# Optimization experiments

Measured on AMD Instinct MI355X. Metric: run time of the kernel, lower is better.

## Reference

```python
import jax, jax.numpy as jnp
import numpy as np

B, S, EMB, HID, IMG, ATT, K, HL = 64, 512, 768, 512, 2048, 512, 6, 20


def setup_inputs() -> dict:
    key = jax.random.key(0)
    ks = jax.random.split(key, 14)
    u = lambda k, shape: jax.random.uniform(k, shape, jnp.float32, -0.1, 0.1)
    return {
        "representations": jax.random.normal(ks[0], (B, S, EMB), jnp.float32),
        "lengths": jax.random.randint(ks[1], (B,), 0, S),
        "separate_images": jax.random.normal(ks[2], (B, K, IMG), jnp.float32),
        "visual_context": jax.random.normal(ks[3], (B, K * IMG), jnp.float32),
        "prev_hist": jax.random.normal(ks[4], (B, K, HL, EMB), jnp.float32),
        "hist_counts": jax.random.randint(ks[5], (B, K), 0, HL + 1),
        "masks": jax.random.randint(ks[6], (B, S, 1), 0, 2).astype(bool),
        "W_sep": u(ks[7], (IMG, HID)), "b_sep": jnp.zeros((HID,), jnp.float32),
        "W_e2h": u(ks[8], (EMB, HID)), "b_e2h": jnp.zeros((HID,), jnp.float32),
        "W_hist": u(ks[9], (EMB, HID)), "b_hist": jnp.zeros((HID,), jnp.float32),
        "W_ctx": u(ks[10], (K * IMG, HID)), "b_ctx": jnp.zeros((HID,), jnp.float32),
        "W_mm": u(ks[11], (2 * HID, HID)), "b_mm": jnp.zeros((HID,), jnp.float32),
        "W_a1": u(ks[12], (HID, ATT)), "b_a1": jnp.zeros((ATT,), jnp.float32),
        "W_a2": u(ks[13], (ATT, 1)), "b_a2": jnp.zeros((1,), jnp.float32),
    }


def reference(representations, lengths, separate_images, visual_context,
              prev_hist, hist_counts, masks,
              W_sep, b_sep, W_e2h, b_e2h, W_hist, b_hist, W_ctx, b_ctx,
              W_mm, b_mm, W_a1, b_a1, W_a2, b_a2):
    # dropout_prob = 0 -> dropout is identity (eval-mode equivalence)
    input_reps = jax.nn.relu(representations @ W_e2h + b_e2h)          # [B,S,H]
    ctx = jax.nn.relu(visual_context @ W_ctx + b_ctx)                  # [B,H]
    ctx_rep = jnp.broadcast_to(ctx[:, None, :], input_reps.shape)
    mm = jax.nn.relu(jnp.concatenate([input_reps, ctx_rep], -1) @ W_mm + b_mm)  # [B,S,H]
    scores = jnp.tanh(mm @ W_a1 + b_a1) @ W_a2 + b_a2                  # [B,S,1]
    scores = jnp.where(masks, -jnp.inf, scores)
    att_w = jax.nn.softmax(scores, axis=1)                             # softmax over seq
    attended = jnp.sum(mm * att_w, axis=1)                             # [B,H]

    sep = separate_images @ W_sep + b_sep                              # [B,K,H]
    hl = prev_hist.shape[2]
    valid = jnp.arange(hl)[None, None, :] < hist_counts[:, :, None]    # [B,K,HL]
    hsum = jnp.sum(prev_hist * valid[..., None].astype(prev_hist.dtype), axis=2)
    havg = hsum / jnp.maximum(hist_counts, 1)[..., None].astype(prev_hist.dtype)
    hproj = jax.nn.relu(havg @ W_hist + b_hist)                        # [B,K,H]
    sep = sep + jnp.where((hist_counts > 0)[..., None], hproj, 0.0)
    sep = jax.nn.relu(sep)
    # F.normalize(p=2, dim=2, eps=1e-12)
    sep = sep / jnp.maximum(jnp.linalg.norm(sep, axis=2, keepdims=True), 1e-12)
    dot = jnp.einsum('bkh,bh->bk', sep, attended)[..., None]           # [B,K,1]
    return dot
```

## Files before the change

### kernel.cpp

```cpp
#include <hip/hip_runtime.h>
#include <math.h>

#define B_    64
#define S_    512
#define EMB_  768
#define HID_  512
#define IMG_  2048
#define ATT_  512
#define K_    6
#define HL_   20
#define MS_   (B_ * S_)

typedef __attribute__((ext_vector_type(8))) short bf16x8;
typedef __attribute__((ext_vector_type(4))) float f32x4;

__device__ __forceinline__ unsigned short f2b(float f) {
    unsigned int u = __float_as_uint(f);
    u += 0x7fffu + ((u >> 16) & 1u);
    return (unsigned short)(u >> 16);
}
__device__ __forceinline__ unsigned int pk_bf16(float lo, float hi) {
    unsigned int r;
    asm volatile("v_cvt_pk_bf16_f32 %0, %1, %2" : "=v"(r) : "v"(lo), "v"(hi));
    return r;
}

#define GLD_LDS16(gp, lp)                                                        \
    __builtin_amdgcn_global_load_lds(                                            \
        (const __attribute__((address_space(1))) void*)(gp),                     \
        (__attribute__((address_space(3))) void*)(lp), 16, 0, 0)

__global__ __launch_bounds__(256)
void prep(const float* __restrict__ W_e2h, const float* __restrict__ W_mm,
          const float* __restrict__ W_a1,
          unsigned short* __restrict__ WtE2H, unsigned short* __restrict__ WtMM,
          unsigned short* __restrict__ WtA1,
          const unsigned char* __restrict__ masks, int* __restrict__ flag) {
    const int z = blockIdx.z;
    if (z == 3) {
        if (blockIdx.x != 0 || blockIdx.y != 0) return;
        __shared__ int found;
        if (threadIdx.x == 0) found = 0;
        __syncthreads();
        for (int i = threadIdx.x; i < 8192; i += 256)
            if ((i & 3) != 0 && masks[i] != 0) found = 1;
        __syncthreads();
        if (threadIdx.x == 0) *flag = found;
        return;
    }
    const float* W;
    unsigned short* Wt;
    int Kd;
    if (z == 0)      { W = W_e2h; Wt = WtE2H; Kd = EMB_; }
    else if (z == 1) { W = W_mm;  Wt = WtMM;  Kd = HID_; }
    else             { W = W_a1;  Wt = WtA1;  Kd = HID_; }
    if ((int)blockIdx.x * 32 >= Kd) return;

    __shared__ float tile[32][33];
    int k0 = blockIdx.x * 32, n0 = blockIdx.y * 32;
    int tx = threadIdx.x & 31, ty = threadIdx.x >> 5;
    #pragma unroll
    for (int i = 0; i < 4; ++i)
        tile[ty + i * 8][tx] = W[(size_t)(k0 + ty + i * 8) * HID_ + n0 + tx];
    __syncthreads();
    #pragma unroll
    for (int i = 0; i < 4; ++i)
        Wt[(size_t)(n0 + ty + i * 8) * Kd + k0 + tx] = f2b(tile[tx][ty + i * 8]);
}

template<bool AF32, int ACT, bool SCORE>
__global__ __launch_bounds__(512)
void gemm256(const void* __restrict__ Av, const unsigned short* __restrict__ Bt,
             const float* __restrict__ bias, const float* __restrict__ row_add,
             int row_div, unsigned short* __restrict__ Co,
             const float* __restrict__ W_a2, float* __restrict__ scores8,
             int M, int N, int Kd) {
    __shared__ unsigned short Als[2][256 * 64];
    __shared__ unsigned short Bls[2][256 * 64];
    const int tid = threadIdx.x;

    const int nwg = gridDim.x;
    const int cpx = nwg >> 3;
    const int lid = ((int)blockIdx.x & 7) * cpx + ((int)blockIdx.x >> 3);
    const int ntl = N >> 8;
    const int bn = (lid % ntl) << 8;
    const int bm = (lid / ntl) << 8;

    const int lane = tid & 63, wid = tid >> 6;
    const int wr = wid >> 2, wc = wid & 3;
    const int fr = lane & 15, hi = lane >> 4;

    const unsigned short* Ab = (const unsigned short*)Av;
    const float* Af = (const float*)Av;

    f32x4 acc[8][4] = {};

    int srow[4], lcol[4], scol[4];
    #pragma unroll
    for (int c = 0; c < 4; ++c) {
        int g = c * 512 + tid;
        srow[c] = g >> 3;
        lcol[c] = g & 7;
        scol[c] = lcol[c] ^ (srow[c] & 7);
    }

    float4 ra[8];

    auto stageA_lds = [&](int t, int buf) {
        #pragma unroll
        for (int c = 0; c < 4; ++c) {
            int g = c * 512 + tid;
            GLD_LDS16(Ab + (size_t)(bm + srow[c]) * Kd + t * 64 + scol[c] * 8,
                      &Als[buf][g * 8]);
        }
    };
    auto stageB_lds = [&](int t, int buf) {
        #pragma unroll
        for (int c = 0; c < 4; ++c) {
            int g = c * 512 + tid;
            GLD_LDS16(Bt + (size_t)(bn + srow[c]) * Kd + t * 64 + scol[c] * 8,
                      &Bls[buf][g * 8]);
        }
    };
    auto loadA = [&](int t) {
        #pragma unroll
        for (int c = 0; c < 4; ++c) {
            const float* p = Af + (size_t)(bm + srow[c]) * Kd + t * 64 + scol[c] * 8;
            ra[2 * c]     = *(const float4*)p;
            ra[2 * c + 1] = *(const float4*)(p + 4);
        }
    };
    auto writeA = [&](int buf) {
        #pragma unroll
        for (int c = 0; c < 4; ++c) {
            int g = c * 512 + tid;
            uint4 u;
            u.x = pk_bf16(ra[2*c].x,   ra[2*c].y);
            u.y = pk_bf16(ra[2*c].z,   ra[2*c].w);
            u.z = pk_bf16(ra[2*c+1].x, ra[2*c+1].y);
            u.w = pk_bf16(ra[2*c+1].z, ra[2*c+1].w);
            *(uint4*)&Als[buf][g * 8] = u;
        }
    };
    auto compute = [&](int buf) {
        #pragma unroll
        for (int kk = 0; kk < 2; ++kk) {
            bf16x8 af[8], bv[4];
            #pragma unroll
            for (int m = 0; m < 8; ++m) {
                int r = wr * 128 + m * 16 + fr;
                int sc = (kk * 4 + hi) ^ (r & 7);
                af[m] = *(const bf16x8*)&Als[buf][r * 64 + sc * 8];
            }
            #pragma unroll
            for (int n = 0; n < 4; ++n) {
                int r = wc * 64 + n * 16 + fr;
                int sc = (kk * 4 + hi) ^ (r & 7);
                bv[n] = *(const bf16x8*)&Bls[buf][r * 64 + sc * 8];
            }
            #pragma unroll
            for (int m = 0; m < 8; ++m)
                #pragma unroll
                for (int n = 0; n < 4; ++n)
                    acc[m][n] = __builtin_amdgcn_mfma_f32_16x16x32_bf16(af[m], bv[n], acc[m][n], 0, 0, 0);
        }
    };

    const int nt = Kd >> 6;

    if constexpr (AF32) {
        loadA(0);
        stageB_lds(0, 0);
        writeA(0);
    } else {
        stageA_lds(0, 0);
        stageB_lds(0, 0);
    }
    __syncthreads();

    for (int t = 0; t < nt; ++t) {
        const int buf = t & 1;
        const bool pf = (t + 1 < nt);
        if (pf) {
            if constexpr (AF32) {
                loadA(t + 1);
                stageB_lds(t + 1, buf ^ 1);
            } else {
                stageA_lds(t + 1, buf ^ 1);
                stageB_lds(t + 1, buf ^ 1);
            }
        }
        compute(buf);
        if constexpr (AF32) {
            if (pf) writeA(buf ^ 1);
        }
        __syncthreads();
    }

    if (SCORE) {
        float ba[4], wa[4];
        #pragma unroll
        for (int n = 0; n < 4; ++n) {
            int col = bn + wc * 64 + n * 16 + fr;
            ba[n] = bias[col];
            wa[n] = W_a2[col];
        }
        const int slot = (bn >> 6) + wc;
        #pragma unroll
        for (int m = 0; m < 8; ++m) {
            #pragma unroll
            for (int r = 0; r < 4; ++r) {
                float p = 0.f;
                #pragma unroll
                for (int n = 0; n < 4; ++n)
                    p += tanhf(acc[m][n][r] + ba[n]) * wa[n];
                p += __shfl_xor(p, 1, 64);
                p += __shfl_xor(p, 2, 64);
                p += __shfl_xor(p, 4, 64);
                p += __shfl_xor(p, 8, 64);
                if (fr == 0)
                    scores8[(size_t)slot * M + bm + wr * 128 + m * 16 + hi * 4 + r] = p;
            }
        }
    } else {
        #pragma unroll
        for (int m = 0; m < 8; ++m) {
            #pragma unroll
            for (int n = 0; n < 4; ++n) {
                int col = bn + wc * 64 + n * 16 + fr;
                float badd = bias ? bias[col] : 0.f;
                #pragma unroll
                for (int r = 0; r < 4; ++r) {
                    int row = bm + wr * 128 + m * 16 + hi * 4 + r;
                    float x = acc[m][n][r] + badd;
                    if (row_add) x += row_add[(size_t)(row / row_div) * N + col];
                    if (ACT == 1) x = fmaxf(x, 0.f);
                    Co[(size_t)row * N + col] = f2b(x);
                }
            }
        }
    }
}

__global__ __launch_bounds__(256)
void gemm_splitk(const float* __restrict__ A, const float* __restrict__ W,
                 float* __restrict__ P, int M, int N, int Kd, int kps) {
    __shared__ float As[16][68];
    __shared__ float Ws[16][64];
    const int tid = threadIdx.x;
    const int bm = blockIdx.y * 64, bn = blockIdx.x * 64;
    const int ks = blockIdx.z;
    const int tx = tid & 15, ty = tid >> 4;
    const int arow = tid >> 2, akq = tid & 3;
    const int wk = tid >> 4, wnq = tid & 15;

    float acc[4][4] = {};
    const int kbeg = ks * kps, kend = kbeg + kps;

    for (int k0 = kbeg; k0 < kend; k0 += 16) {
        float4 av = *(const float4*)&A[(size_t)(bm + arow) * Kd + k0 + akq * 4];
        float4 wv = *(const float4*)&W[(size_t)(k0 + wk) * N + bn + wnq * 4];
        As[akq * 4 + 0][arow] = av.x;
        As[akq * 4 + 1][arow] = av.y;
        As[akq * 4 + 2][arow] = av.z;
        As[akq * 4 + 3][arow] = av.w;
        *(float4*)&Ws[wk][wnq * 4] = wv;
        __syncthreads();
        #pragma unroll
        for (int kk = 0; kk < 16; ++kk) {
            float4 a4 = *(const float4*)&As[kk][ty * 4];
            float4 b4 = *(const float4*)&Ws[kk][tx * 4];
            float a_[4] = {a4.x, a4.y, a4.z, a4.w};
            float b_[4] = {b4.x, b4.y, b4.z, b4.w};
            #pragma unroll
            for (int i = 0; i < 4; ++i)
                #pragma unroll
                for (int j = 0; j < 4; ++j)
                    acc[i][j] += a_[i] * b_[j];
        }
        __syncthreads();
    }

    float* Pbase = P + (size_t)ks * M * N;
    #pragma unroll
    for (int i = 0; i < 4; ++i) {
        int row = bm + ty * 4 + i;
        float4 v = {acc[i][0], acc[i][1], acc[i][2], acc[i][3]};
        *(float4*)&Pbase[(size_t)row * N + bn + tx * 4] = v;
    }
}

template<int ACT>
__global__ __launch_bounds__(256)
void reduce_k(const float* __restrict__ P, const float* __restrict__ bias,
              float* __restrict__ C, int MN, int N, int nsplit) {
    int idx = blockIdx.x * 256 + threadIdx.x;
    if (idx >= MN) return;
    float s = 0.f;
    for (int z = 0; z < nsplit; ++z) s += P[(size_t)z * MN + idx];
    if (bias) s += bias[idx & (N - 1)];
    if (ACT == 1) s = fmaxf(s, 0.f);
    C[idx] = s;
}

__global__ __launch_bounds__(256)
void softmax8(const float* __restrict__ scores8, const float* __restrict__ b_a2,
              const void* __restrict__ masks_raw, const int* __restrict__ flag,
              float* __restrict__ attw) {
    int b = blockIdx.x, tid = threadIdx.x;
    bool isb = (*flag) != 0;
    const unsigned char* mb = (const unsigned char*)masks_raw;
    const int* mi = (const int*)masks_raw;
    int lane = tid & 63, wv = tid >> 6;
    __shared__ float red[4], red2[4];
    float bias = b_a2[0];

    float m = -INFINITY;
    for (int s = tid; s < S_; s += 256) {
        int idx = b * S_ + s;
        float v = bias;
        #pragma unroll
        for (int z = 0; z < 8; ++z) v += scores8[(size_t)z * MS_ + idx];
        bool mk = isb ? (mb[idx] != 0) : (mi[idx] != 0);
        v = mk ? -INFINITY : v;
        attw[idx] = v;
        m = fmaxf(m, v);
    }
    #pragma unroll
    for (int off = 32; off; off >>= 1) m = fmaxf(m, __shfl_down(m, off, 64));
    if (lane == 0) red[wv] = m;
    __syncthreads();
    if (tid == 0) red[0] = fmaxf(fmaxf(red[0], red[1]), fmaxf(red[2], red[3]));
    __syncthreads();
    float Mx = red[0];

    float sum = 0.f;
    for (int s = tid; s < S_; s += 256) {
        int idx = b * S_ + s;
        float e = expf(attw[idx] - Mx);
        attw[idx] = e;
        sum += e;
    }
    #pragma unroll
    for (int off = 32; off; off >>= 1) sum += __shfl_down(sum, off, 64);
    if (lane == 0) red2[wv] = sum;
    __syncthreads();
    if (tid == 0) red2[0] = red2[0] + red2[1] + red2[2] + red2[3];
    __syncthreads();
    float inv = 1.f / red2[0];
    for (int s = tid; s < S_; s += 256) attw[b * S_ + s] *= inv;
}

__global__ __launch_bounds__(256)
void attended4(const unsigned short* __restrict__ mm, const float* __restrict__ attw,
               float* __restrict__ att4) {
    int b = blockIdx.x, z = blockIdx.y;
    int h2 = threadIdx.x;
    __shared__ float w[128];
    int s0 = z * 128;
    if (threadIdx.x < 128) w[threadIdx.x] = attw[b * S_ + s0 + threadIdx.x];
    __syncthreads();
    const unsigned int* base =
        (const unsigned int*)mm + ((size_t)b * S_ + s0) * (HID_ / 2) + h2;
    float a0 = 0.f, a1 = 0.f;
    for (int s = 0; s < 128; ++s) {
        unsigned int u = base[(size_t)s * (HID_ / 2)];
        a0 += __uint_as_float(u << 16) * w[s];
        a1 += __uint_as_float(u & 0xffff0000u) * w[s];
    }
    float2 r = {a0, a1};
    *(float2*)&att4[((size_t)z * B_ + b) * HID_ + h2 * 2] = r;
}

__global__ __launch_bounds__(256)
void hist_avg(const float* __restrict__ ph, const int* __restrict__ hcnt,
              float* __restrict__ havg) {
    int bk = blockIdx.x;
    int cnt = hcnt[bk];
    float denom = (float)(cnt > 1 ? cnt : 1);
    const float* base = ph + (size_t)bk * HL_ * EMB_;
    for (int e = threadIdx.x; e < EMB_; e += 256) {
        float s = 0.f;
        for (int l = 0; l < cnt; ++l) s += base[l * EMB_ + e];
        havg[bk * EMB_ + e] = s / denom;
    }
}

__global__ __launch_bounds__(256)
void combine_all(const float* __restrict__ skA, const float* __restrict__ skB,
                 const float* __restrict__ b_hist, const float* __restrict__ b_sep,
                 const int* __restrict__ hcnt, const float* __restrict__ att4,
                 float* __restrict__ out) {
    const int MNA = B_ * K_ * HID_;
    int bk = blockIdx.x, tid = threadIdx.x;
    int b = bk / K_;
    int cnt = hcnt[bk];
    float sq = 0.f, dt = 0.f;
    #pragma unroll
    for (int i = 0; i < HID_ / 256; ++i) {
        int h = tid + i * 256;
        size_t idx = (size_t)bk * HID_ + h;
        float hp = b_hist[h];
        #pragma unroll
        for (int z = 0; z < 8; ++z) hp += skA[(size_t)z * MNA + idx];
        hp = fmaxf(hp, 0.f);
        float sp = b_sep[h];
        #pragma unroll
        for (int z = 0; z < 16; ++z) sp += skB[(size_t)z * MNA + idx];
        float v = sp + (cnt > 0 ? hp : 0.f);
        v = fmaxf(v, 0.f);
        float at = 0.f;
        #pragma unroll
        for (int z = 0; z < 4; ++z) at += att4[((size_t)z * B_ + b) * HID_ + h];
        sq += v * v;
        dt += v * at;
    }
    #pragma unroll
    for (int off = 32; off; off >>= 1) {
        sq += __shfl_down(sq, off, 64);
        dt += __shfl_down(dt, off, 64);
    }
    __shared__ float rs[4], rd[4];
    int lane = tid & 63, wv = tid >> 6;
    if (lane == 0) { rs[wv] = sq; rd[wv] = dt; }
    __syncthreads();
    if (tid == 0) {
        float Sq = rs[0] + rs[1] + rs[2] + rs[3];
        float Dt = rd[0] + rd[1] + rd[2] + rd[3];
        float norm = fmaxf(sqrtf(Sq), 1e-12f);
        out[bk] = Dt / norm;
    }
}

extern "C" void kernel_launch(void* const* d_in, const int* in_sizes, int n_in,
                              void* d_out, int out_size, void* d_ws, size_t ws_size,
                              hipStream_t stream) {
    const float* reps     = (const float*)d_in[0];
    const float* sep_imgs = (const float*)d_in[2];
    const float* vctx     = (const float*)d_in[3];
    const float* phist    = (const float*)d_in[4];
    const int*   hcnt     = (const int*)d_in[5];
    const void*  masks    = d_in[6];
    const float* W_sep = (const float*)d_in[7];
    const float* b_sep = (const float*)d_in[8];
    const float* W_e2h = (const float*)d_in[9];
    const float* b_e2h = (const float*)d_in[10];
    const float* W_hist = (const float*)d_in[11];
    const float* b_hist = (const float*)d_in[12];
    const float* W_ctx = (const float*)d_in[13];
    const float* b_ctx = (const float*)d_in[14];
    const float* W_mm = (const float*)d_in[15];
    const float* b_mm = (const float*)d_in[16];
    const float* W_a1 = (const float*)d_in[17];
    const float* b_a1 = (const float*)d_in[18];
    const float* W_a2 = (const float*)d_in[19];
    const float* b_a2 = (const float*)d_in[20];
    float* out = (float*)d_out;

    const size_t MS = (size_t)MS_;
    const int MNA = B_ * K_ * HID_;

    unsigned short* actA  = (unsigned short*)d_ws;
    unsigned short* actB  = actA + MS * HID_;
    unsigned short* WtE2H = actB + MS * HID_;
    unsigned short* WtMM  = WtE2H + (size_t)EMB_ * HID_;
    unsigned short* WtA1  = WtMM + (size_t)HID_ * HID_;
    float* skC    = (float*)(WtA1 + (size_t)HID_ * HID_);
    float* skA    = skC + (size_t)64 * B_ * HID_;
    float* skB    = skA + (size_t)8 * MNA;
    float* scores8 = skB + (size_t)16 * MNA;
    float* attw   = scores8 + 8 * MS;
    float* att4   = attw + MS;
    float* ctx    = att4 + (size_t)4 * B_ * HID_;
    float* ctx2   = ctx + B_ * HID_;
    float* havg   = ctx2 + B_ * HID_;
    int*   flag   = (int*)(havg + (size_t)B_ * K_ * EMB_);

    prep<<<dim3(EMB_ / 32, HID_ / 32, 4), 256, 0, stream>>>(
        W_e2h, W_mm, W_a1, WtE2H, WtMM, WtA1, (const unsigned char*)masks, flag);

    {
        const int nsp = 64, kps = (K_ * IMG_) / nsp;
        gemm_splitk<<<dim3(8, 1, nsp), 256, 0, stream>>>(vctx, W_ctx, skC,
                                                         B_, HID_, K_ * IMG_, kps);
        reduce_k<1><<<(B_ * HID_ + 255) / 256, 256, 0, stream>>>(skC, b_ctx, ctx,
                                                                 B_ * HID_, HID_, nsp);
    }
    {
        const int nsp = 8, kps = HID_ / nsp;
        gemm_splitk<<<dim3(8, 1, nsp), 256, 0, stream>>>(ctx, W_mm + (size_t)HID_ * HID_,
                                                         skC, B_, HID_, HID_, kps);
        reduce_k<0><<<(B_ * HID_ + 255) / 256, 256, 0, stream>>>(skC, b_mm, ctx2,
                                                                 B_ * HID_, HID_, nsp);
    }

    const int big_grid = (MS_ / 256) * (HID_ / 256);
    gemm256<true, 1, false><<<big_grid, 512, 0, stream>>>(
        reps, WtE2H, b_e2h, nullptr, 1, actA, nullptr, nullptr, MS_, HID_, EMB_);
    gemm256<false, 1, false><<<big_grid, 512, 0, stream>>>(
        actA, WtMM, nullptr, ctx2, S_, actB, nullptr, nullptr, MS_, HID_, HID_);
    gemm256<false, 0, true><<<big_grid, 512, 0, stream>>>(
        actB, WtA1, b_a1, nullptr, 1, actA, W_a2, scores8, MS_, ATT_, HID_);
    softmax8<<<B_, 256, 0, stream>>>(scores8, b_a2, masks, flag, attw);
    attended4<<<dim3(B_, 4), 256, 0, stream>>>(actB, attw, att4);
    hist_avg<<<B_ * K_, 256, 0, stream>>>(phist, hcnt, havg);
    gemm_splitk<<<dim3(8, 6, 8), 256, 0, stream>>>(havg, W_hist, skA,
                                                   B_ * K_, HID_, EMB_, EMB_ / 8);
    gemm_splitk<<<dim3(8, 6, 16), 256, 0, stream>>>(sep_imgs, W_sep, skB,
                                                    B_ * K_, HID_, IMG_, IMG_ / 16);
    combine_all<<<B_ * K_, 256, 0, stream>>>(skA, skB, b_hist, b_sep, hcnt,
                                             att4, out);
}
```

Measured before the change: 262.3 us.

## Shrink GEMM tiles to 128x128 and read B fragments directly from global

```diff
diff --git a/kernel.cpp b/kernel.cpp
--- a/kernel.cpp
+++ b/kernel.cpp
@@ -68,58 +68,56 @@
         Wt[(size_t)(n0 + ty + i * 8) * Kd + k0 + tx] = f2b(tile[tx][ty + i * 8]);
 }
 
-template<bool AF32, int ACT, bool SCORE>
-__global__ __launch_bounds__(512)
-void gemm256(const void* __restrict__ Av, const unsigned short* __restrict__ Bt,
-             const float* __restrict__ bias, const float* __restrict__ row_add,
-             int row_div, unsigned short* __restrict__ Co,
-             const float* __restrict__ W_a2, float* __restrict__ scores8,
-             int M, int N, int Kd) {
-    __shared__ unsigned short Als[2][256 * 64];
-    __shared__ unsigned short Bls[2][256 * 64];
-    const int tid = threadIdx.x;
-
+__device__ __forceinline__ void tile_coords(int N, int& bm, int& bn) {
     const int nwg = gridDim.x;
     const int cpx = nwg >> 3;
     const int lid = ((int)blockIdx.x & 7) * cpx + ((int)blockIdx.x >> 3);
-    const int ntl = N >> 8;
-    const int bn = (lid % ntl) << 8;
-    const int bm = (lid / ntl) << 8;
-
+    const int ntl = N >> 7;
+    bn = (lid % ntl) << 7;
+    bm = (lid / ntl) << 7;
+}
+
+template<bool AF32, int ACT, bool SCORE>
+__global__ __launch_bounds__(256)
+void gemm_bdir(const void* __restrict__ Av, const unsigned short* __restrict__ Bt,
+               const float* __restrict__ bias, const float* __restrict__ row_add,
+               int row_div, unsigned short* __restrict__ Co,
+               const float* __restrict__ W_a2, float* __restrict__ scores8,
+               int M, int N, int Kd) {
+    __shared__ unsigned short Als[2][128 * 64];
+    const int tid = threadIdx.x;
+    int bm, bn; tile_coords(N, bm, bn);
     const int lane = tid & 63, wid = tid >> 6;
-    const int wr = wid >> 2, wc = wid & 3;
+    const int wr = wid >> 1, wc = wid & 1;
     const int fr = lane & 15, hi = lane >> 4;
 
     const unsigned short* Ab = (const unsigned short*)Av;
     const float* Af = (const float*)Av;
 
-    f32x4 acc[8][4] = {};
+    f32x4 acc[4][4] = {};
 
     int srow[4], lcol[4], scol[4];
     #pragma unroll
     for (int c = 0; c < 4; ++c) {
-        int g = c * 512 + tid;
+        int g = c * 256 + tid;
         srow[c] = g >> 3;
         lcol[c] = g & 7;
         scol[c] = lcol[c] ^ (srow[c] & 7);
     }
 
+    const unsigned short* pB[4];
+    #pragma unroll
+    for (int n = 0; n < 4; ++n)
+        pB[n] = Bt + (size_t)(bn + wc * 64 + n * 16 + fr) * Kd + hi * 8;
+
     float4 ra[8];
 
     auto stageA_lds = [&](int t, int buf) {
         #pragma unroll
         for (int c = 0; c < 4; ++c) {
-            int g = c * 512 + tid;
+            int g = c * 256 + tid;
             GLD_LDS16(Ab + (size_t)(bm + srow[c]) * Kd + t * 64 + scol[c] * 8,
                       &Als[buf][g * 8]);
-        }
-    };
-    auto stageB_lds = [&](int t, int buf) {
-        #pragma unroll
-        for (int c = 0; c < 4; ++c) {
-            int g = c * 512 + tid;
-            GLD_LDS16(Bt + (size_t)(bn + srow[c]) * Kd + t * 64 + scol[c] * 8,
-                      &Bls[buf][g * 8]);
         }
     };
     auto loadA = [&](int t) {
@@ -133,7 +131,7 @@
     auto writeA = [&](int buf) {
         #pragma unroll
         for (int c = 0; c < 4; ++c) {
-            int g = c * 512 + tid;
+            int g = c * 256 + tid;
             uint4 u;
             u.x = pk_bf16(ra[2*c].x,   ra[2*c].y);
             u.y = pk_bf16(ra[2*c].z,   ra[2*c].w);
@@ -142,24 +140,21 @@
             *(uint4*)&Als[buf][g * 8] = u;
         }
     };
-    auto compute = [&](int buf) {
+    auto compute = [&](int buf, int t) {
         #pragma unroll
         for (int kk = 0; kk < 2; ++kk) {
-            bf16x8 af[8], bv[4];
+            bf16x8 af[4], bv[4];
             #pragma unroll
-            for (int m = 0; m < 8; ++m) {
-                int r = wr * 128 + m * 16 + fr;
-                int sc = (kk * 4 + hi) ^ (r & 7);
+            for (int n = 0; n < 4; ++n)
+                bv[n] = *(const bf16x8*)(pB[n] + t * 64 + kk * 32);
+            #pragma unroll
+            for (int m = 0; m < 4; ++m) {
+                int r = wr * 64 + m * 16 + fr;
+                int sc = (kk * 4 + hi) ^ (fr & 7);
                 af[m] = *(const bf16x8*)&Als[buf][r * 64 + sc * 8];
             }
             #pragma unroll
-            for (int n = 0; n < 4; ++n) {
-                int r = wc * 64 + n * 16 + fr;
-                int sc = (kk * 4 + hi) ^ (r & 7);
-                bv[n] = *(const bf16x8*)&Bls[buf][r * 64 + sc * 8];
-            }
-            #pragma unroll
-            for (int m = 0; m < 8; ++m)
+            for (int m = 0; m < 4; ++m)
                 #pragma unroll
                 for (int n = 0; n < 4; ++n)
                     acc[m][n] = __builtin_amdgcn_mfma_f32_16x16x32_bf16(af[m], bv[n], acc[m][n], 0, 0, 0);
@@ -170,11 +165,9 @@
 
     if constexpr (AF32) {
         loadA(0);
-        stageB_lds(0, 0);
         writeA(0);
     } else {
         stageA_lds(0, 0);
-        stageB_lds(0, 0);
     }
     __syncthreads();
 
@@ -182,15 +175,10 @@
         const int buf = t & 1;
         const bool pf = (t + 1 < nt);
         if (pf) {
-            if constexpr (AF32) {
-                loadA(t + 1);
-                stageB_lds(t + 1, buf ^ 1);
-            } else {
-                stageA_lds(t + 1, buf ^ 1);
-                stageB_lds(t + 1, buf ^ 1);
-            }
-        }
-        compute(buf);
+            if constexpr (AF32) loadA(t + 1);
+            else                stageA_lds(t + 1, buf ^ 1);
+        }
+        compute(buf, t);
         if constexpr (AF32) {
             if (pf) writeA(buf ^ 1);
         }
@@ -205,9 +193,9 @@
             ba[n] = bias[col];
             wa[n] = W_a2[col];
         }
-        const int slot = (bn >> 6) + wc;
-        #pragma unroll
-        for (int m = 0; m < 8; ++m) {
+        const int slot = (bn >> 7) * 2 + wc;
+        #pragma unroll
+        for (int m = 0; m < 4; ++m) {
             #pragma unroll
             for (int r = 0; r < 4; ++r) {
                 float p = 0.f;
@@ -219,19 +207,19 @@
                 p += __shfl_xor(p, 4, 64);
                 p += __shfl_xor(p, 8, 64);
                 if (fr == 0)
-                    scores8[(size_t)slot * M + bm + wr * 128 + m * 16 + hi * 4 + r] = p;
+                    scores8[(size_t)slot * M + bm + wr * 64 + m * 16 + hi * 4 + r] = p;
             }
         }
     } else {
         #pragma unroll
-        for (int m = 0; m < 8; ++m) {
+        for (int m = 0; m < 4; ++m) {
             #pragma unroll
             for (int n = 0; n < 4; ++n) {
                 int col = bn + wc * 64 + n * 16 + fr;
                 float badd = bias ? bias[col] : 0.f;
                 #pragma unroll
                 for (int r = 0; r < 4; ++r) {
-                    int row = bm + wr * 128 + m * 16 + hi * 4 + r;
+                    int row = bm + wr * 64 + m * 16 + hi * 4 + r;
                     float x = acc[m][n][r] + badd;
                     if (row_add) x += row_add[(size_t)(row / row_div) * N + col];
                     if (ACT == 1) x = fmaxf(x, 0.f);
@@ -494,12 +482,12 @@
                                                                  B_ * HID_, HID_, nsp);
     }
 
-    const int big_grid = (MS_ / 256) * (HID_ / 256);
-    gemm256<true, 1, false><<<big_grid, 512, 0, stream>>>(
+    const int big_grid = (MS_ / 128) * (HID_ / 128);
+    gemm_bdir<true, 1, false><<<big_grid, 256, 0, stream>>>(
         reps, WtE2H, b_e2h, nullptr, 1, actA, nullptr, nullptr, MS_, HID_, EMB_);
-    gemm256<false, 1, false><<<big_grid, 512, 0, stream>>>(
+    gemm_bdir<false, 1, false><<<big_grid, 256, 0, stream>>>(
         actA, WtMM, nullptr, ctx2, S_, actB, nullptr, nullptr, MS_, HID_, HID_);
-    gemm256<false, 0, true><<<big_grid, 512, 0, stream>>>(
+    gemm_bdir<false, 0, true><<<big_grid, 256, 0, stream>>>(
         actB, WtA1, b_a1, nullptr, 1, actA, W_a2, scores8, MS_, ATT_, HID_);
     softmax8<<<B_, 256, 0, stream>>>(scores8, b_a2, masks, flag, attw);
     attended4<<<dim3(B_, 4), 256, 0, stream>>>(actB, attw, att4);
```

New measurement: 317.6 us. 1.21x slower.
